# Kernel optimization log

Measured on AMD Instinct MI355X. Metric: run time of the kernel, lower is better.

The kernel has to match this reference:

```python
import jax, jax.numpy as jnp
import numpy as np
from jax import lax

M, T, WINDOW = 4096, 2048, 25
NEG_DIAG = -1e10  # matches alphas.fill_diagonal_(-1e10)


def setup_inputs() -> dict:
    key = jax.random.key(0)
    k_ys, k_a, k_r, k_b0, k_b1 = jax.random.split(key, 5)
    ys = jax.random.uniform(k_ys, (M, T), dtype=jnp.float32) * 10.0  # case counts
    alphas = 0.01 * jax.random.normal(k_a, (M, M), dtype=jnp.float32)
    repro = 1.0 + 0.01 * jax.random.normal(k_r, (M, WINDOW), dtype=jnp.float32)  # init ones
    b0 = 0.1 * jax.random.normal(k_b0, (M, 1), dtype=jnp.float32)
    b1 = 0.01 * jax.random.normal(k_b1, (M, 1), dtype=jnp.float32)
    t = jnp.arange(T, dtype=jnp.int32) + 1
    return {"ys": ys, "alphas": alphas, "repro": repro, "b0": b0, "b1": b1, "t": t}


def reference(ys, alphas, repro, b0, b1, t):
    m, _ = ys.shape
    window = repro.shape[1]
    offset = window - 1
    # metapopulation weights: sigmoid adjacency with diagonal forced to ~0
    diag = jnp.eye(m, dtype=bool)
    W = jax.nn.sigmoid(jnp.where(diag, jnp.asarray(NEG_DIAG, ys.dtype), alphas))
    # depthwise conv1d (cross-correlation), groups=M, VALID padding -> (M, T-window+1)
    Z = lax.conv_general_dilated(
        ys[None],                 # (1, M, T)
        repro[:, None, :],        # (M, 1, window)
        window_strides=(1,),
        padding='VALID',
        feature_group_count=m,
        dimension_numbers=('NCH', 'OIH', 'NCH'),
    )[0]                          # (M, T')
    ys_n = ys[:, offset:]         # (M, T')
    # beta_net: per-node softplus-linear in time -> (M, T), then narrow
    tt = t.astype(ys.dtype)
    beta = jax.nn.softplus(b0 + b1 * tt[None, :])[:, offset:]  # (M, T')
    return beta * (jax.nn.softplus(Z) + W @ ys_n)
```

## Files before the change

### kernel.cpp

```cpp
#include <hip/hip_runtime.h>
#include <stdint.h>

#define M_DIM 4096
#define T_DIM 2048
#define N_OUT 2024
#define N_PAD 2048
#define WIN   25
#define K_DIM 4096

typedef short bf16x8 __attribute__((ext_vector_type(8)));
typedef float f32x4  __attribute__((ext_vector_type(4)));

__device__ __forceinline__ unsigned short f2bf(float x) {
  unsigned u = __float_as_uint(x);
  u += 0x7FFF + ((u >> 16) & 1);
  return (unsigned short)(u >> 16);
}
__device__ __forceinline__ float bf2f(unsigned short h) {
  return __uint_as_float(((unsigned)h) << 16);
}

__device__ __forceinline__ void gl2lds16(const void* g, void* l) {
  __builtin_amdgcn_global_load_lds(
      (const __attribute__((address_space(1))) unsigned int*)g,
      (__attribute__((address_space(3))) unsigned int*)l, 16, 0, 0);
}

__global__ __launch_bounds__(256) void k_wcast(const float* __restrict__ alphas,
                                               unsigned short* __restrict__ Wb) {
  size_t i8 = ((size_t)blockIdx.x * 256 + threadIdx.x) * 8;
  const float4 v0 = *(const float4*)(alphas + i8);
  const float4 v1 = *(const float4*)(alphas + i8 + 4);
  int row = (int)(i8 >> 12);
  int col = (int)(i8 & 4095);
  float a[8] = {v0.x, v0.y, v0.z, v0.w, v1.x, v1.y, v1.z, v1.w};
  ushort4 o[2];
  unsigned short* op = (unsigned short*)o;
#pragma unroll
  for (int j = 0; j < 8; ++j) {
    float w = (row == col + j) ? 0.f : 1.f / (1.f + __expf(-a[j]));
    op[j] = f2bf(w);
  }
  *(uint4*)(Wb + i8) = *(uint4*)o;
}

__global__ __launch_bounds__(256) void k_conv(const float* __restrict__ ys,
                                              const float* __restrict__ repro,
                                              unsigned short* __restrict__ Sbf) {
  __shared__ float sy[256 + WIN - 1];
  __shared__ float sr[WIN];
  int m = blockIdx.y;
  int j0 = blockIdx.x * 256;
  int tid = threadIdx.x;
  sy[tid] = ys[(size_t)m * T_DIM + j0 + tid];
  if (tid < WIN - 1) {
    int jj = j0 + 256 + tid;
    sy[256 + tid] = (jj < T_DIM) ? ys[(size_t)m * T_DIM + jj] : 0.f;
  }
  if (tid < WIN) sr[tid] = repro[m * WIN + tid];
  __syncthreads();
  int j = j0 + tid;
  float z = 0.f;
#pragma unroll
  for (int k = 0; k < WIN; ++k) z += sy[tid + k] * sr[k];
  float sp = fmaxf(z, 0.f) + log1pf(__expf(-fabsf(z)));
  Sbf[(size_t)m * N_PAD + j] = (j < N_OUT) ? f2bf(sp) : (unsigned short)0;
}

__global__ __launch_bounds__(256) void k_transpose(const float* __restrict__ ys,
                                                   unsigned short* __restrict__ BT) {
  __shared__ float t[64][65];
  int n0 = blockIdx.x * 64;
  int k0 = blockIdx.y * 64;
  int tx = threadIdx.x;
  int ty = threadIdx.y;
#pragma unroll
  for (int r = 0; r < 16; ++r) {
    int kk = k0 + ty + r * 4;
    int n = n0 + tx;
    t[ty + r * 4][tx] = (n < N_OUT) ? ys[(size_t)kk * T_DIM + n + (WIN - 1)] : 0.f;
  }
  __syncthreads();
#pragma unroll
  for (int r = 0; r < 16; ++r) {
    int n = n0 + ty + r * 4;
    int kk = k0 + tx;
    BT[(size_t)n * K_DIM + kk] = f2bf(t[tx][ty + r * 4]);
  }
}

__global__ __launch_bounds__(256) void k_gemm(const unsigned short* __restrict__ Wb,
                                              const unsigned short* __restrict__ BT,
                                              const unsigned short* __restrict__ Sbf,
                                              const float* __restrict__ b0,
                                              const float* __restrict__ b1,
                                              float* __restrict__ out) {
  __shared__ __align__(16) unsigned short lA[128 * 32];
  __shared__ __align__(16) unsigned short lB[128 * 32];
  const int tid  = threadIdx.x;
  const int wave = tid >> 6;
  const int lane = tid & 63;
  const int wm = wave >> 1, wn = wave & 1;
  const int m16  = lane & 15;
  const int quad = lane >> 4;
  const int tileM = blockIdx.y * 128;
  const int tileN = blockIdx.x * 128;

  const int swz   = ((quad ^ ((m16 >> 1) & 3)) << 4);
  const int offA0 = (wm * 64 + m16) * 64 + swz;
  const int offB0 = (wn * 64 + m16) * 64 + swz;

  const char* gA[2];
  const char* gB[2];
  char* ldsA[2];
  char* ldsB[2];
#pragma unroll
  for (int c = 0; c < 2; ++c) {
    int o  = c * 4096 + wave * 1024 + lane * 16;
    int r  = o >> 6;
    int cc = (o >> 4) & 3;
    int q  = cc ^ ((r >> 1) & 3);
    gA[c] = (const char*)Wb + (((size_t)(tileM + r) * K_DIM) << 1) + q * 16;
    gB[c] = (const char*)BT + (((size_t)(tileN + r) * K_DIM) << 1) + q * 16;
    ldsA[c] = (char*)lA + c * 4096 + wave * 1024;
    ldsB[c] = (char*)lB + c * 4096 + wave * 1024;
  }

  f32x4 acc[4][4];
#pragma unroll
  for (int i = 0; i < 4; ++i)
#pragma unroll
    for (int j = 0; j < 4; ++j) acc[i][j] = f32x4{0.f, 0.f, 0.f, 0.f};

  for (int kt = 0; kt < K_DIM / 32; ++kt) {
    const size_t kb = (size_t)kt * 64;
#pragma unroll
    for (int c = 0; c < 2; ++c) {
      gl2lds16(gA[c] + kb, ldsA[c]);
      gl2lds16(gB[c] + kb, ldsB[c]);
    }
    __syncthreads();
    bf16x8 aF[4], bF[4];
#pragma unroll
    for (int i = 0; i < 4; ++i) {
      aF[i] = *(const bf16x8*)((const char*)lA + offA0 + i * 1024);
      bF[i] = *(const bf16x8*)((const char*)lB + offB0 + i * 1024);
    }
#pragma unroll
    for (int i = 0; i < 4; ++i)
#pragma unroll
      for (int j = 0; j < 4; ++j)
        acc[i][j] = __builtin_amdgcn_mfma_f32_16x16x32_bf16(aF[i], bF[j], acc[i][j], 0, 0, 0);
    __syncthreads();
  }

#pragma unroll
  for (int j = 0; j < 4; ++j) {
    int gn = tileN + wn * 64 + j * 16 + m16;
    if (gn >= N_OUT) continue;
    float tval = (float)(gn + WIN);
#pragma unroll
    for (int i = 0; i < 4; ++i) {
#pragma unroll
      for (int r = 0; r < 4; ++r) {
        int gm = tileM + wm * 64 + i * 16 + quad * 4 + r;
        float x = b0[gm] + b1[gm] * tval;
        float beta = fmaxf(x, 0.f) + log1pf(__expf(-fabsf(x)));
        float s = bf2f(Sbf[(size_t)gm * N_PAD + gn]);
        out[(size_t)gm * N_OUT + gn] = beta * (s + acc[i][j][r]);
      }
    }
  }
}

extern "C" void kernel_launch(void* const* d_in, const int* in_sizes, int n_in,
                              void* d_out, int out_size, void* d_ws, size_t ws_size,
                              hipStream_t stream) {
  const float* ys     = (const float*)d_in[0];
  const float* alphas = (const float*)d_in[1];
  const float* repro  = (const float*)d_in[2];
  const float* b0     = (const float*)d_in[3];
  const float* b1     = (const float*)d_in[4];
  float* out = (float*)d_out;

  char* ws = (char*)d_ws;
  unsigned short* Wb  = (unsigned short*)ws;
  unsigned short* BT  = (unsigned short*)(ws + (size_t)M_DIM * K_DIM * 2);
  unsigned short* Sbf = (unsigned short*)(ws + (size_t)M_DIM * K_DIM * 2
                                             + (size_t)N_PAD * K_DIM * 2);

  k_wcast<<<(M_DIM * (size_t)K_DIM) / 8 / 256, 256, 0, stream>>>(alphas, Wb);
  k_conv<<<dim3(T_DIM / 256, M_DIM), 256, 0, stream>>>(ys, repro, Sbf);
  k_transpose<<<dim3(N_PAD / 64, K_DIM / 64), dim3(64, 4), 0, stream>>>(ys, BT);
  k_gemm<<<dim3(N_PAD / 128, M_DIM / 128), 256, 0, stream>>>(Wb, BT, Sbf, b0, b1, out);
}
```

Baseline: 287.9 us.

## Double-buffer LDS tiles in the bf16 MFMA GEMM to overlap loads with compute

Splits the GEMM's A and B shared-memory tiles into two buffers. The main loop now issues the async global-to-LDS loads for the next K-slice before running the MFMAs on the current slice, and the loop is unrolled by two. The aim is to hide global load latency behind matrix math instead of stalling at a barrier before every compute step. The cost is twice the LDS per block, which may reduce occupancy.

New measurement: 297.5 us. 3.3% more time.

```diff
diff --git a/kernel.cpp b/kernel.cpp
--- a/kernel.cpp
+++ b/kernel.cpp
@@ -95,8 +95,8 @@
                                               const float* __restrict__ b0,
                                               const float* __restrict__ b1,
                                               float* __restrict__ out) {
-  __shared__ __align__(16) unsigned short lA[128 * 32];
-  __shared__ __align__(16) unsigned short lB[128 * 32];
+  __shared__ __align__(16) unsigned short lA[2][128 * 32];
+  __shared__ __align__(16) unsigned short lB[2][128 * 32];
   const int tid  = threadIdx.x;
   const int wave = tid >> 6;
   const int lane = tid & 63;
@@ -112,8 +112,7 @@
 
   const char* gA[2];
   const char* gB[2];
-  char* ldsA[2];
-  char* ldsB[2];
+  int ldsOff[2];
 #pragma unroll
   for (int c = 0; c < 2; ++c) {
     int o  = c * 4096 + wave * 1024 + lane * 16;
@@ -122,8 +121,7 @@
     int q  = cc ^ ((r >> 1) & 3);
     gA[c] = (const char*)Wb + (((size_t)(tileM + r) * K_DIM) << 1) + q * 16;
     gB[c] = (const char*)BT + (((size_t)(tileN + r) * K_DIM) << 1) + q * 16;
-    ldsA[c] = (char*)lA + c * 4096 + wave * 1024;
-    ldsB[c] = (char*)lB + c * 4096 + wave * 1024;
+    ldsOff[c] = c * 4096 + wave * 1024;
   }
 
   f32x4 acc[4][4];
@@ -132,27 +130,44 @@
 #pragma unroll
     for (int j = 0; j < 4; ++j) acc[i][j] = f32x4{0.f, 0.f, 0.f, 0.f};
 
-  for (int kt = 0; kt < K_DIM / 32; ++kt) {
-    const size_t kb = (size_t)kt * 64;
-#pragma unroll
-    for (int c = 0; c < 2; ++c) {
-      gl2lds16(gA[c] + kb, ldsA[c]);
-      gl2lds16(gB[c] + kb, ldsB[c]);
-    }
+#define STAGE(buf, kt_)                                              \
+  {                                                                  \
+    const size_t kb = (size_t)(kt_) * 64;                            \
+    _Pragma("unroll")                                                \
+    for (int c = 0; c < 2; ++c) {                                    \
+      gl2lds16(gA[c] + kb, (char*)lA[buf] + ldsOff[c]);              \
+      gl2lds16(gB[c] + kb, (char*)lB[buf] + ldsOff[c]);              \
+    }                                                                \
+  }
+
+#define COMPUTE(buf)                                                 \
+  {                                                                  \
+    bf16x8 aF[4], bF[4];                                             \
+    _Pragma("unroll")                                                \
+    for (int i = 0; i < 4; ++i) {                                    \
+      aF[i] = *(const bf16x8*)((const char*)lA[buf] + offA0 + i * 1024); \
+      bF[i] = *(const bf16x8*)((const char*)lB[buf] + offB0 + i * 1024); \
+    }                                                                \
+    _Pragma("unroll")                                                \
+    for (int i = 0; i < 4; ++i)                                      \
+      _Pragma("unroll")                                              \
+      for (int j = 0; j < 4; ++j)                                    \
+        acc[i][j] = __builtin_amdgcn_mfma_f32_16x16x32_bf16(         \
+            aF[i], bF[j], acc[i][j], 0, 0, 0);                       \
+  }
+
+  STAGE(0, 0)
+  __syncthreads();
+  for (int kt = 0; kt < K_DIM / 32; kt += 2) {
+    STAGE(1, kt + 1)
+    COMPUTE(0)
     __syncthreads();
-    bf16x8 aF[4], bF[4];
-#pragma unroll
-    for (int i = 0; i < 4; ++i) {
-      aF[i] = *(const bf16x8*)((const char*)lA + offA0 + i * 1024);
-      bF[i] = *(const bf16x8*)((const char*)lB + offB0 + i * 1024);
-    }
-#pragma unroll
-    for (int i = 0; i < 4; ++i)
-#pragma unroll
-      for (int j = 0; j < 4; ++j)
-        acc[i][j] = __builtin_amdgcn_mfma_f32_16x16x32_bf16(aF[i], bF[j], acc[i][j], 0, 0, 0);
+    if (kt + 2 < K_DIM / 32) STAGE(0, kt + 2)
+    COMPUTE(1)
     __syncthreads();
   }
+#undef STAGE
+#undef COMPUTE
 
 #pragma unroll
   for (int j = 0; j < 4; ++j) {
```

## Split GEMM K dimension in two and reduce partials in separate epilogue kernel

Applied to the files above, without the earlier changes.

The GEMM grid gains a z dimension of 2, and each half accumulates over half of K. Half 0 writes fp32 partials directly into the output, and half 1 writes bf16 partials to a new workspace buffer. A new epilogue kernel sums the two partials, adds the conv softplus term and multiplies by beta. This doubles the block count from 512 to 1024 to better fill the GPU's CUs, at the cost of extra global traffic, an extra launch and bf16 rounding of one partial sum.

After: 301.7 us. 1.05x slower.

```diff
diff --git a/kernel.cpp b/kernel.cpp
--- a/kernel.cpp
+++ b/kernel.cpp
@@ -91,9 +91,7 @@
 
 __global__ __launch_bounds__(256) void k_gemm(const unsigned short* __restrict__ Wb,
                                               const unsigned short* __restrict__ BT,
-                                              const unsigned short* __restrict__ Sbf,
-                                              const float* __restrict__ b0,
-                                              const float* __restrict__ b1,
+                                              unsigned short* __restrict__ Cp1,
                                               float* __restrict__ out) {
   __shared__ __align__(16) unsigned short lA[128 * 32];
   __shared__ __align__(16) unsigned short lB[128 * 32];
@@ -105,6 +103,7 @@
   const int quad = lane >> 4;
   const int tileM = blockIdx.y * 128;
   const int tileN = blockIdx.x * 128;
+  const int kz    = blockIdx.z;
 
   const int swz   = ((quad ^ ((m16 >> 1) & 3)) << 4);
   const int offA0 = (wm * 64 + m16) * 64 + swz;
@@ -132,7 +131,9 @@
 #pragma unroll
     for (int j = 0; j < 4; ++j) acc[i][j] = f32x4{0.f, 0.f, 0.f, 0.f};
 
-  for (int kt = 0; kt < K_DIM / 32; ++kt) {
+  const int ktBeg = kz * (K_DIM / 64);
+  const int ktEnd = ktBeg + (K_DIM / 64);
+  for (int kt = ktBeg; kt < ktEnd; ++kt) {
     const size_t kb = (size_t)kt * 64;
 #pragma unroll
     for (int c = 0; c < 2; ++c) {
@@ -154,23 +155,60 @@
     __syncthreads();
   }
 
-#pragma unroll
-  for (int j = 0; j < 4; ++j) {
-    int gn = tileN + wn * 64 + j * 16 + m16;
-    if (gn >= N_OUT) continue;
-    float tval = (float)(gn + WIN);
-#pragma unroll
-    for (int i = 0; i < 4; ++i) {
-#pragma unroll
-      for (int r = 0; r < 4; ++r) {
-        int gm = tileM + wm * 64 + i * 16 + quad * 4 + r;
-        float x = b0[gm] + b1[gm] * tval;
-        float beta = fmaxf(x, 0.f) + log1pf(__expf(-fabsf(x)));
-        float s = bf2f(Sbf[(size_t)gm * N_PAD + gn]);
-        out[(size_t)gm * N_OUT + gn] = beta * (s + acc[i][j][r]);
-      }
-    }
-  }
+  if (kz == 0) {
+#pragma unroll
+    for (int j = 0; j < 4; ++j) {
+      int gn = tileN + wn * 64 + j * 16 + m16;
+      if (gn >= N_OUT) continue;
+#pragma unroll
+      for (int i = 0; i < 4; ++i)
+#pragma unroll
+        for (int r = 0; r < 4; ++r) {
+          int gm = tileM + wm * 64 + i * 16 + quad * 4 + r;
+          out[(size_t)gm * N_OUT + gn] = acc[i][j][r];
+        }
+    }
+  } else {
+#pragma unroll
+    for (int j = 0; j < 4; ++j) {
+      int gn = tileN + wn * 64 + j * 16 + m16;
+#pragma unroll
+      for (int i = 0; i < 4; ++i)
+#pragma unroll
+        for (int r = 0; r < 4; ++r) {
+          int gm = tileM + wm * 64 + i * 16 + quad * 4 + r;
+          Cp1[(size_t)gm * N_PAD + gn] = f2bf(acc[i][j][r]);
+        }
+    }
+  }
+}
+
+__global__ __launch_bounds__(256) void k_epi(const unsigned short* __restrict__ Cp1,
+                                             const unsigned short* __restrict__ Sbf,
+                                             const float* __restrict__ b0,
+                                             const float* __restrict__ b1,
+                                             float* __restrict__ out) {
+  int row = blockIdx.x;
+  int c8  = threadIdx.x * 8;
+  if (c8 >= N_OUT) return;
+  float vb0 = b0[row], vb1 = b1[row];
+  uint4 p1 = *(const uint4*)(Cp1 + (size_t)row * N_PAD + c8);
+  uint4 sv = *(const uint4*)(Sbf + (size_t)row * N_PAD + c8);
+  const unsigned short* p1s = (const unsigned short*)&p1;
+  const unsigned short* svs = (const unsigned short*)&sv;
+  float* orow = out + (size_t)row * N_OUT + c8;
+  float4 o0 = *(const float4*)orow;
+  float4 o1 = *(const float4*)(orow + 4);
+  float oc[8] = {o0.x, o0.y, o0.z, o0.w, o1.x, o1.y, o1.z, o1.w};
+  float res[8];
+#pragma unroll
+  for (int e = 0; e < 8; ++e) {
+    float x = vb0 + vb1 * (float)(c8 + e + WIN);
+    float beta = fmaxf(x, 0.f) + log1pf(__expf(-fabsf(x)));
+    res[e] = beta * (bf2f(svs[e]) + oc[e] + bf2f(p1s[e]));
+  }
+  *(float4*)orow = float4{res[0], res[1], res[2], res[3]};
+  *(float4*)(orow + 4) = float4{res[4], res[5], res[6], res[7]};
 }
 
 extern "C" void kernel_launch(void* const* d_in, const int* in_sizes, int n_in,
@@ -188,9 +226,13 @@
   unsigned short* BT  = (unsigned short*)(ws + (size_t)M_DIM * K_DIM * 2);
   unsigned short* Sbf = (unsigned short*)(ws + (size_t)M_DIM * K_DIM * 2
                                              + (size_t)N_PAD * K_DIM * 2);
+  unsigned short* Cp1 = (unsigned short*)(ws + (size_t)M_DIM * K_DIM * 2
+                                             + (size_t)N_PAD * K_DIM * 2
+                                             + (size_t)M_DIM * N_PAD * 2);
 
   k_wcast<<<(M_DIM * (size_t)K_DIM) / 8 / 256, 256, 0, stream>>>(alphas, Wb);
   k_conv<<<dim3(T_DIM / 256, M_DIM), 256, 0, stream>>>(ys, repro, Sbf);
   k_transpose<<<dim3(N_PAD / 64, K_DIM / 64), dim3(64, 4), 0, stream>>>(ys, BT);
-  k_gemm<<<dim3(N_PAD / 128, M_DIM / 128), 256, 0, stream>>>(Wb, BT, Sbf, b0, b1, out);
-}
+  k_gemm<<<dim3(N_PAD / 128, M_DIM / 128, 2), 256, 0, stream>>>(Wb, BT, Cp1, out);
+  k_epi<<<M_DIM, 256, 0, stream>>>(Cp1, Sbf, b0, b1, out);
+}
```

## Switch weight-sum GEMM operands from bf16 to fp8 MFMA

Applied to the files above, without the earlier changes.

Casts the sigmoid weight matrix and the transposed ys slice to fp8 (e4m3) instead of bf16, and runs the GEMM with 16x16x32 fp8 MFMA over 64-wide K tiles. This halves operand bytes in the preprocessing writes and the GEMM loads, and halves the number of K-loop iterations and barriers. The transpose now writes 16-byte packed rows. The cost is much coarser precision: ys values up to 10 and the sigmoid weights lose mantissa bits, which risks exceeding the accuracy tolerance on a 4096-long reduction.

Result: faster. 263.8 us (-8.4%).

```diff
diff --git a/kernel.cpp b/kernel.cpp
--- a/kernel.cpp
+++ b/kernel.cpp
@@ -8,8 +8,7 @@
 #define WIN   25
 #define K_DIM 4096
 
-typedef short bf16x8 __attribute__((ext_vector_type(8)));
-typedef float f32x4  __attribute__((ext_vector_type(4)));
+typedef float f32x4 __attribute__((ext_vector_type(4)));
 
 __device__ __forceinline__ unsigned short f2bf(float x) {
   unsigned u = __float_as_uint(x);
@@ -26,22 +25,27 @@
       (__attribute__((address_space(3))) unsigned int*)l, 16, 0, 0);
 }
 
+__device__ __forceinline__ int pk_fp8x4(float a, float b, float c, float d) {
+  int w = __builtin_amdgcn_cvt_pk_fp8_f32(a, b, 0, false);
+  w = __builtin_amdgcn_cvt_pk_fp8_f32(c, d, w, true);
+  return w;
+}
+
 __global__ __launch_bounds__(256) void k_wcast(const float* __restrict__ alphas,
-                                               unsigned short* __restrict__ Wb) {
+                                               unsigned char* __restrict__ W8) {
   size_t i8 = ((size_t)blockIdx.x * 256 + threadIdx.x) * 8;
   const float4 v0 = *(const float4*)(alphas + i8);
   const float4 v1 = *(const float4*)(alphas + i8 + 4);
   int row = (int)(i8 >> 12);
   int col = (int)(i8 & 4095);
   float a[8] = {v0.x, v0.y, v0.z, v0.w, v1.x, v1.y, v1.z, v1.w};
-  ushort4 o[2];
-  unsigned short* op = (unsigned short*)o;
-#pragma unroll
-  for (int j = 0; j < 8; ++j) {
-    float w = (row == col + j) ? 0.f : 1.f / (1.f + __expf(-a[j]));
-    op[j] = f2bf(w);
-  }
-  *(uint4*)(Wb + i8) = *(uint4*)o;
+  float w[8];
+#pragma unroll
+  for (int j = 0; j < 8; ++j)
+    w[j] = (row == col + j) ? 0.f : 1.f / (1.f + __expf(-a[j]));
+  int p0 = pk_fp8x4(w[0], w[1], w[2], w[3]);
+  int p1 = pk_fp8x4(w[4], w[5], w[6], w[7]);
+  *(uint2*)(W8 + i8) = uint2{(unsigned)p0, (unsigned)p1};
 }
 
 __global__ __launch_bounds__(256) void k_conv(const float* __restrict__ ys,
@@ -68,7 +72,7 @@
 }
 
 __global__ __launch_bounds__(256) void k_transpose(const float* __restrict__ ys,
-                                                   unsigned short* __restrict__ BT) {
+                                                   unsigned char* __restrict__ BT8) {
   __shared__ float t[64][65];
   int n0 = blockIdx.x * 64;
   int k0 = blockIdx.y * 64;
@@ -81,22 +85,26 @@
     t[ty + r * 4][tx] = (n < N_OUT) ? ys[(size_t)kk * T_DIM + n + (WIN - 1)] : 0.f;
   }
   __syncthreads();
-#pragma unroll
-  for (int r = 0; r < 16; ++r) {
-    int n = n0 + ty + r * 4;
-    int kk = k0 + tx;
-    BT[(size_t)n * K_DIM + kk] = f2bf(t[tx][ty + r * 4]);
-  }
-}
-
-__global__ __launch_bounds__(256) void k_gemm(const unsigned short* __restrict__ Wb,
-                                              const unsigned short* __restrict__ BT,
+  int tid = ty * 64 + tx;
+  int nl = tid >> 2;
+  int kc = (tid & 3) * 16;
+  unsigned wds[4];
+#pragma unroll
+  for (int w = 0; w < 4; ++w)
+    wds[w] = (unsigned)pk_fp8x4(t[kc + 4 * w][nl], t[kc + 4 * w + 1][nl],
+                                t[kc + 4 * w + 2][nl], t[kc + 4 * w + 3][nl]);
+  *(uint4*)(BT8 + (size_t)(n0 + nl) * K_DIM + k0 + kc) =
+      uint4{wds[0], wds[1], wds[2], wds[3]};
+}
+
+__global__ __launch_bounds__(256) void k_gemm(const unsigned char* __restrict__ W8,
+                                              const unsigned char* __restrict__ BT8,
                                               const unsigned short* __restrict__ Sbf,
                                               const float* __restrict__ b0,
                                               const float* __restrict__ b1,
                                               float* __restrict__ out) {
-  __shared__ __align__(16) unsigned short lA[128 * 32];
-  __shared__ __align__(16) unsigned short lB[128 * 32];
+  __shared__ __align__(16) unsigned char lA[128 * 64];
+  __shared__ __align__(16) unsigned char lB[128 * 64];
   const int tid  = threadIdx.x;
   const int wave = tid >> 6;
   const int lane = tid & 63;
@@ -106,24 +114,29 @@
   const int tileM = blockIdx.y * 128;
   const int tileN = blockIdx.x * 128;
 
-  const int swz   = ((quad ^ ((m16 >> 1) & 3)) << 4);
-  const int offA0 = (wm * 64 + m16) * 64 + swz;
-  const int offB0 = (wn * 64 + m16) * 64 + swz;
-
-  const char* gA[2];
-  const char* gB[2];
-  char* ldsA[2];
-  char* ldsB[2];
+  const int key  = (m16 >> 1) & 3;
+  const int sub  = (quad & 1) * 8;
+  const int rowA = (wm * 64 + m16) * 64;
+  const int rowB = (wn * 64 + m16) * 64;
+  int hOf[2];
+#pragma unroll
+  for (int h = 0; h < 2; ++h)
+    hOf[h] = (((2 * h + (quad >> 1)) ^ key) << 4) + sub;
+
+  const unsigned char* gA[2];
+  const unsigned char* gB[2];
+  unsigned char* ldsA[2];
+  unsigned char* ldsB[2];
 #pragma unroll
   for (int c = 0; c < 2; ++c) {
     int o  = c * 4096 + wave * 1024 + lane * 16;
     int r  = o >> 6;
-    int cc = (o >> 4) & 3;
-    int q  = cc ^ ((r >> 1) & 3);
-    gA[c] = (const char*)Wb + (((size_t)(tileM + r) * K_DIM) << 1) + q * 16;
-    gB[c] = (const char*)BT + (((size_t)(tileN + r) * K_DIM) << 1) + q * 16;
-    ldsA[c] = (char*)lA + c * 4096 + wave * 1024;
-    ldsB[c] = (char*)lB + c * 4096 + wave * 1024;
+    int s  = (o >> 4) & 3;
+    int q  = s ^ ((r >> 1) & 3);
+    gA[c] = W8  + (size_t)(tileM + r) * K_DIM + q * 16;
+    gB[c] = BT8 + (size_t)(tileN + r) * K_DIM + q * 16;
+    ldsA[c] = lA + c * 4096 + wave * 1024;
+    ldsB[c] = lB + c * 4096 + wave * 1024;
   }
 
   f32x4 acc[4][4];
@@ -132,7 +145,7 @@
 #pragma unroll
     for (int j = 0; j < 4; ++j) acc[i][j] = f32x4{0.f, 0.f, 0.f, 0.f};
 
-  for (int kt = 0; kt < K_DIM / 32; ++kt) {
+  for (int kt = 0; kt < K_DIM / 64; ++kt) {
     const size_t kb = (size_t)kt * 64;
 #pragma unroll
     for (int c = 0; c < 2; ++c) {
@@ -140,17 +153,21 @@
       gl2lds16(gB[c] + kb, ldsB[c]);
     }
     __syncthreads();
-    bf16x8 aF[4], bF[4];
-#pragma unroll
-    for (int i = 0; i < 4; ++i) {
-      aF[i] = *(const bf16x8*)((const char*)lA + offA0 + i * 1024);
-      bF[i] = *(const bf16x8*)((const char*)lB + offB0 + i * 1024);
+#pragma unroll
+    for (int h = 0; h < 2; ++h) {
+      long long aF[4], bF[4];
+#pragma unroll
+      for (int i = 0; i < 4; ++i) {
+        aF[i] = *(const long long*)(lA + rowA + i * 1024 + hOf[h]);
+        bF[i] = *(const long long*)(lB + rowB + i * 1024 + hOf[h]);
+      }
+#pragma unroll
+      for (int i = 0; i < 4; ++i)
+#pragma unroll
+        for (int j = 0; j < 4; ++j)
+          acc[i][j] = __builtin_amdgcn_mfma_f32_16x16x32_fp8_fp8(
+              aF[i], bF[j], acc[i][j], 0, 0, 0);
     }
-#pragma unroll
-    for (int i = 0; i < 4; ++i)
-#pragma unroll
-      for (int j = 0; j < 4; ++j)
-        acc[i][j] = __builtin_amdgcn_mfma_f32_16x16x32_bf16(aF[i], bF[j], acc[i][j], 0, 0, 0);
     __syncthreads();
   }
 
@@ -184,13 +201,13 @@
   float* out = (float*)d_out;
 
   char* ws = (char*)d_ws;
-  unsigned short* Wb  = (unsigned short*)ws;
-  unsigned short* BT  = (unsigned short*)(ws + (size_t)M_DIM * K_DIM * 2);
-  unsigned short* Sbf = (unsigned short*)(ws + (size_t)M_DIM * K_DIM * 2
-                                             + (size_t)N_PAD * K_DIM * 2);
-
-  k_wcast<<<(M_DIM * (size_t)K_DIM) / 8 / 256, 256, 0, stream>>>(alphas, Wb);
+  unsigned char*  W8  = (unsigned char*)ws;
+  unsigned char*  BT8 = (unsigned char*)(ws + (size_t)M_DIM * K_DIM);
+  unsigned short* Sbf = (unsigned short*)(ws + (size_t)M_DIM * K_DIM
+                                             + (size_t)N_PAD * K_DIM);
+
+  k_wcast<<<(M_DIM * (size_t)K_DIM) / 8 / 256, 256, 0, stream>>>(alphas, W8);
   k_conv<<<dim3(T_DIM / 256, M_DIM), 256, 0, stream>>>(ys, repro, Sbf);
-  k_transpose<<<dim3(N_PAD / 64, K_DIM / 64), dim3(64, 4), 0, stream>>>(ys, BT);
-  k_gemm<<<dim3(N_PAD / 128, M_DIM / 128), 256, 0, stream>>>(Wb, BT, Sbf, b0, b1, out);
-}
+  k_transpose<<<dim3(N_PAD / 64, K_DIM / 64), dim3(64, 4), 0, stream>>>(ys, BT8);
+  k_gemm<<<dim3(N_PAD / 128, M_DIM / 128), 256, 0, stream>>>(W8, BT8, Sbf, b0, b1, out);
+}
```
